# Performance work log

Hardware: AMD Instinct MI355X
Metric: run time of the kernel (lower is better)

The kernel has to match this reference:

```python
import jax, jax.numpy as jnp
import numpy as np

ALPHA = 1.0  # default alpha in the torch forward


def local_patches(x, patch_size):
    """Replicates F.unfold(kernel=p, pad=p//2, stride=1) for x of shape [N,1,H,W].
    Returns [N, p*p, H, W]; patch index is row-major over (kh, kw), matching
    torch.unfold's channel-major/kernel row-major layout (C=1 here)."""
    N, C, H, W = x.shape
    pad = patch_size // 2
    xp = jnp.pad(x, ((0, 0), (0, 0), (pad, pad), (pad, pad)))
    # fixed small loop over the p*p kernel offsets (p=3 -> 9 slices)
    shifts = [xp[:, :, i:i + H, j:j + W]
              for i in range(patch_size) for j in range(patch_size)]
    return jnp.concatenate(shifts, axis=1)  # [N, p*p, H, W]


def setup_inputs() -> dict:
    key = jax.random.key(0)
    x_rgb = jax.random.uniform(key, (8, 3, 512, 512), dtype=jnp.float32)
    return {"x_rgb": x_rgb, "patch_size": 3}


def reference(x_rgb, patch_size):
    # scale_factor=1 -> interpolate is identity
    r = x_rgb[:, 0:1]  # [N,1,H,W]
    g = x_rgb[:, 1:2]
    b = x_rgb[:, 2:3]
    l_channel = 0.2126 * r + 0.7152 * g + 0.0722 * b

    local_r = local_patches(r, patch_size)  # [N,9,H,W]
    local_g = local_patches(g, patch_size)
    local_b = local_patches(b, patch_size)
    local_l = 0.2126 * local_r + 0.7152 * local_g + 0.0722 * local_b

    local_difference_l = (local_l - l_channel) ** 2
    correlation = jax.nn.softmax(-local_difference_l / ALPHA, axis=1)  # [N,9,H,W]

    out_r = jnp.sum(correlation * local_r, axis=1, keepdims=True)
    out_g = jnp.sum(correlation * local_g, axis=1, keepdims=True)
    out_b = jnp.sum(correlation * local_b, axis=1, keepdims=True)
    return jnp.concatenate((out_r, out_g, out_b), axis=1)  # [N,3,H,W]
```

## Files before the change

### kernel.cpp

```cpp
#include <hip/hip_runtime.h>


#define HH 512
#define WW 512
#define HWSZ (HH * WW)

__global__ __launch_bounds__(256) void wavg_kernel(const float* __restrict__ x,
                                                   float* __restrict__ out,
                                                   int total ) {
    int idx = blockIdx.x * 256 + threadIdx.x;
    if (idx >= total) return;

    int n   = idx >> 18;
    int rem = idx & (HWSZ - 1);
    int h   = rem >> 9;
    int w   = rem & (WW - 1);

    const float* Rp = x + (size_t)n * 3 * HWSZ;
    const float* Gp = Rp + HWSZ;
    const float* Bp = Gp + HWSZ;

    float rc = Rp[rem], gc = Gp[rem], bc = Bp[rem];
    float lc = 0.2126f * rc + 0.7152f * gc + 0.0722f * bc;

    float sw = 0.f, sr = 0.f, sg = 0.f, sb = 0.f;

#pragma unroll
    for (int dy = -1; dy <= 1; ++dy) {
#pragma unroll
        for (int dx = -1; dx <= 1; ++dx) {
            int hh = h + dy, ww = w + dx;
            bool inb = ((unsigned)hh < HH) & ((unsigned)ww < WW);
            int i2 = (hh << 9) + ww;
            float rn = 0.f, gn = 0.f, bn = 0.f;
            if (inb) {
                rn = Rp[i2];
                gn = Gp[i2];
                bn = Bp[i2];
            }
            float ln = 0.2126f * rn + 0.7152f * gn + 0.0722f * bn;
            float d  = ln - lc;
            float wt = __expf(-d * d);
            sw += wt;
            sr += wt * rn;
            sg += wt * gn;
            sb += wt * bn;
        }
    }

    float inv = __builtin_amdgcn_rcpf(sw);
    float* Orp = out + (size_t)n * 3 * HWSZ;
    Orp[rem]            = sr * inv;
    Orp[rem + HWSZ]     = sg * inv;
    Orp[rem + 2 * HWSZ] = sb * inv;
}

extern "C" void kernel_launch(void* const* d_in, const int* in_sizes, int n_in,
                              void* d_out, int out_size, void* d_ws, size_t ws_size,
                              hipStream_t stream) {
    const float* x = (const float*)d_in[0];
    float* out = (float*)d_out;
    int total = in_sizes[0] / 3;
    int blocks = (total + 255) / 256;
    wavg_kernel<<<blocks, 256, 0, stream>>>(x, out, total);
}
```

Before: 21.58 us.

## Process eight pixels per thread with row-wise float4 loads and lane shuffles

Each wave now handles one full image row, with each thread computing eight consecutive pixels. The thread loads the three neighbouring rows with vectorized float4 loads and gets its left and right halo pixels from adjacent lanes through shuffles. Luma is computed once per loaded pixel and reused across the overlapping 3x3 windows, and outputs are written with float4 stores. This cuts per-pixel scalar load instructions and redundant luma math, but raises register use and cuts the thread count eightfold.

After: 34.14 us. 1.58x slower.

```diff
diff --git a/kernel.cpp b/kernel.cpp
--- a/kernel.cpp
+++ b/kernel.cpp
@@ -5,54 +5,97 @@
 #define WW 512
 #define HWSZ (HH * WW)
 
+__device__ __forceinline__ float luma(float r, float g, float b) {
+    return 0.2126f * r + 0.7152f * g + 0.0722f * b;
+}
+
 __global__ __launch_bounds__(256) void wavg_kernel(const float* __restrict__ x,
-                                                   float* __restrict__ out,
-                                                   int total ) {
-    int idx = blockIdx.x * 256 + threadIdx.x;
-    if (idx >= total) return;
+                                                   float* __restrict__ out) {
+    const int lane = threadIdx.x & 63;
+    const int wid  = threadIdx.x >> 6;
+    const int row  = (blockIdx.x << 2) + wid;
+    const int n    = row >> 9;
+    const int h    = row & (HH - 1);
+    const int w0   = lane << 3;
 
-    int n   = idx >> 18;
-    int rem = idx & (HWSZ - 1);
-    int h   = rem >> 9;
-    int w   = rem & (WW - 1);
+    const float* __restrict__ base = x + (size_t)n * 3 * HWSZ;
 
-    const float* Rp = x + (size_t)n * 3 * HWSZ;
-    const float* Gp = Rp + HWSZ;
-    const float* Bp = Gp + HWSZ;
+    float sw[8], sr[8], sg[8], sb[8], lc[8];
+#pragma unroll
+    for (int i = 0; i < 8; ++i) { sw[i] = 0.f; sr[i] = 0.f; sg[i] = 0.f; sb[i] = 0.f; }
 
-    float rc = Rp[rem], gc = Gp[rem], bc = Bp[rem];
-    float lc = 0.2126f * rc + 0.7152f * gc + 0.0722f * bc;
+    auto do_row = [&](int hh, bool set_lc) {
+        const bool inb = (unsigned)hh < HH;
+        const float* Rp = base + (inb ? hh : 0) * WW + w0;
+        const float4 z = make_float4(0.f, 0.f, 0.f, 0.f);
+        float4 r0 = inb ? *(const float4*)(Rp)              : z;
+        float4 r1 = inb ? *(const float4*)(Rp + 4)          : z;
+        float4 g0 = inb ? *(const float4*)(Rp + HWSZ)       : z;
+        float4 g1 = inb ? *(const float4*)(Rp + HWSZ + 4)   : z;
+        float4 b0 = inb ? *(const float4*)(Rp + 2*HWSZ)     : z;
+        float4 b1 = inb ? *(const float4*)(Rp + 2*HWSZ + 4) : z;
 
-    float sw = 0.f, sr = 0.f, sg = 0.f, sb = 0.f;
+        float rr[10], gg[10], bb[10], ll[10];
+        rr[1]=r0.x; rr[2]=r0.y; rr[3]=r0.z; rr[4]=r0.w;
+        rr[5]=r1.x; rr[6]=r1.y; rr[7]=r1.z; rr[8]=r1.w;
+        gg[1]=g0.x; gg[2]=g0.y; gg[3]=g0.z; gg[4]=g0.w;
+        gg[5]=g1.x; gg[6]=g1.y; gg[7]=g1.z; gg[8]=g1.w;
+        bb[1]=b0.x; bb[2]=b0.y; bb[3]=b0.z; bb[4]=b0.w;
+        bb[5]=b1.x; bb[6]=b1.y; bb[7]=b1.z; bb[8]=b1.w;
+
+        float rL = __shfl_up(r1.w, 1);   if (lane == 0)  rL = 0.f;
+        float gL = __shfl_up(g1.w, 1);   if (lane == 0)  gL = 0.f;
+        float bL = __shfl_up(b1.w, 1);   if (lane == 0)  bL = 0.f;
+        float rR = __shfl_down(r0.x, 1); if (lane == 63) rR = 0.f;
+        float gR = __shfl_down(g0.x, 1); if (lane == 63) gR = 0.f;
+        float bR = __shfl_down(b0.x, 1); if (lane == 63) bR = 0.f;
+        rr[0] = rL; gg[0] = gL; bb[0] = bL;
+        rr[9] = rR; gg[9] = gR; bb[9] = bR;
 
 #pragma unroll
-    for (int dy = -1; dy <= 1; ++dy) {
+        for (int t = 0; t < 10; ++t) ll[t] = luma(rr[t], gg[t], bb[t]);
+
+        if (set_lc) {
 #pragma unroll
-        for (int dx = -1; dx <= 1; ++dx) {
-            int hh = h + dy, ww = w + dx;
-            bool inb = ((unsigned)hh < HH) & ((unsigned)ww < WW);
-            int i2 = (hh << 9) + ww;
-            float rn = 0.f, gn = 0.f, bn = 0.f;
-            if (inb) {
-                rn = Rp[i2];
-                gn = Gp[i2];
-                bn = Bp[i2];
+            for (int i = 0; i < 8; ++i) lc[i] = ll[i + 1];
+        }
+
+#pragma unroll
+        for (int i = 0; i < 8; ++i) {
+#pragma unroll
+            for (int t = i; t < i + 3; ++t) {
+                float d  = ll[t] - lc[i];
+                float wt = __expf(-d * d);
+                sw[i] += wt;
+                sr[i] += wt * rr[t];
+                sg[i] += wt * gg[t];
+                sb[i] += wt * bb[t];
             }
-            float ln = 0.2126f * rn + 0.7152f * gn + 0.0722f * bn;
-            float d  = ln - lc;
-            float wt = __expf(-d * d);
-            sw += wt;
-            sr += wt * rn;
-            sg += wt * gn;
-            sb += wt * bn;
         }
-    }
+    };
 
-    float inv = __builtin_amdgcn_rcpf(sw);
-    float* Orp = out + (size_t)n * 3 * HWSZ;
-    Orp[rem]            = sr * inv;
-    Orp[rem + HWSZ]     = sg * inv;
-    Orp[rem + 2 * HWSZ] = sb * inv;
+    do_row(h, true);
+    do_row(h - 1, false);
+    do_row(h + 1, false);
+
+    float inv[8];
+#pragma unroll
+    for (int i = 0; i < 8; ++i) inv[i] = __builtin_amdgcn_rcpf(sw[i]);
+
+    float* Op = out + (size_t)n * 3 * HWSZ + h * WW + w0;
+    float4 o0, o1;
+    o0.x = sr[0]*inv[0]; o0.y = sr[1]*inv[1]; o0.z = sr[2]*inv[2]; o0.w = sr[3]*inv[3];
+    o1.x = sr[4]*inv[4]; o1.y = sr[5]*inv[5]; o1.z = sr[6]*inv[6]; o1.w = sr[7]*inv[7];
+    *(float4*)(Op)     = o0;
+    *(float4*)(Op + 4) = o1;
+    o0.x = sg[0]*inv[0]; o0.y = sg[1]*inv[1]; o0.z = sg[2]*inv[2]; o0.w = sg[3]*inv[3];
+    o1.x = sg[4]*inv[4]; o1.y = sg[5]*inv[5]; o1.z = sg[6]*inv[6]; o1.w = sg[7]*inv[7];
+    *(float4*)(Op + HWSZ)     = o0;
+    *(float4*)(Op + HWSZ + 4) = o1;
+    o0.x = sb[0]*inv[0]; o0.y = sb[1]*inv[1]; o0.z = sb[2]*inv[2]; o0.w = sb[3]*inv[3];
+    o1.x = sb[4]*inv[4]; o1.y = sb[5]*inv[5]; o1.z = sb[6]*inv[6]; o1.w = sb[7]*inv[7];
+    *(float4*)(Op + 2*HWSZ)     = o0;
+    *(float4*)(Op + 2*HWSZ + 4) = o1;
 }
 
 extern "C" void kernel_launch(void* const* d_in, const int* in_sizes, int n_in,
@@ -60,7 +103,8 @@
                               hipStream_t stream) {
     const float* x = (const float*)d_in[0];
     float* out = (float*)d_out;
-    int total = in_sizes[0] / 3;
-    int blocks = (total + 255) / 256;
-    wavg_kernel<<<blocks, 256, 0, stream>>>(x, out, total);
+    int nimg   = in_sizes[0] / (3 * HWSZ);
+    int rows   = nimg * HH;
+    int blocks = rows / 4;
+    wavg_kernel<<<blocks, 256, 0, stream>>>(x, out);
 }
```

## Compute four horizontal pixels per thread with vectorized row loads and stores

Applied to the files above, without the earlier changes.

Each thread now handles four adjacent pixels in a row. It loads a float4 plus two halo scalars for each of three rows and three channels, then reuses those loaded neighbours across the four outputs. Results are written as float4 nontemporal stores. The aim is fewer load instructions and less redundant neighbour traffic per pixel, at the cost of more registers per thread and a quarter as many threads. Boundary handling moves from branches to clamped indices with multiplicative masks.

Result: faster. 20.65 us, median of 2 (-4.3%).

```diff
diff --git a/kernel.cpp b/kernel.cpp
--- a/kernel.cpp
+++ b/kernel.cpp
@@ -5,54 +5,106 @@
 #define WW 512
 #define HWSZ (HH * WW)
 
-__global__ __launch_bounds__(256) void wavg_kernel(const float* __restrict__ x,
-                                                   float* __restrict__ out,
-                                                   int total ) {
-    int idx = blockIdx.x * 256 + threadIdx.x;
-    if (idx >= total) return;
+typedef float f32x4 __attribute__((ext_vector_type(4)));
 
-    int n   = idx >> 18;
-    int rem = idx & (HWSZ - 1);
-    int h   = rem >> 9;
-    int w   = rem & (WW - 1);
+__device__ __forceinline__ float luma(float r, float g, float b) {
+    return 0.2126f * r + 0.7152f * g + 0.0722f * b;
+}
 
-    const float* Rp = x + (size_t)n * 3 * HWSZ;
-    const float* Gp = Rp + HWSZ;
-    const float* Bp = Gp + HWSZ;
+__device__ __forceinline__ void load6(const float* __restrict__ p, int w0,
+                                      int wlC, int wrC, float m, float mL,
+                                      float mR, float o[6]) {
+    f32x4 v  = *(const f32x4*)(p + w0);
+    float lv = p[wlC];
+    float rv = p[wrC];
+    o[0] = lv * mL;
+    o[1] = v.x * m; o[2] = v.y * m; o[3] = v.z * m; o[4] = v.w * m;
+    o[5] = rv * mR;
+}
 
-    float rc = Rp[rem], gc = Gp[rem], bc = Bp[rem];
-    float lc = 0.2126f * rc + 0.7152f * gc + 0.0722f * bc;
-
-    float sw = 0.f, sr = 0.f, sg = 0.f, sb = 0.f;
-
+__device__ __forceinline__ void accum(const float rr[6], const float gg[6],
+                                      const float bb[6], const float lc[4],
+                                      float sw[4], float sr[4], float sg[4],
+                                      float sb[4]) {
+    float ll[6];
 #pragma unroll
-    for (int dy = -1; dy <= 1; ++dy) {
+    for (int t = 0; t < 6; ++t) ll[t] = luma(rr[t], gg[t], bb[t]);
 #pragma unroll
-        for (int dx = -1; dx <= 1; ++dx) {
-            int hh = h + dy, ww = w + dx;
-            bool inb = ((unsigned)hh < HH) & ((unsigned)ww < WW);
-            int i2 = (hh << 9) + ww;
-            float rn = 0.f, gn = 0.f, bn = 0.f;
-            if (inb) {
-                rn = Rp[i2];
-                gn = Gp[i2];
-                bn = Bp[i2];
-            }
-            float ln = 0.2126f * rn + 0.7152f * gn + 0.0722f * bn;
-            float d  = ln - lc;
+    for (int i = 0; i < 4; ++i) {
+#pragma unroll
+        for (int t = i; t < i + 3; ++t) {
+            float d  = ll[t] - lc[i];
             float wt = __expf(-d * d);
-            sw += wt;
-            sr += wt * rn;
-            sg += wt * gn;
-            sb += wt * bn;
+            sw[i] += wt;
+            sr[i] += wt * rr[t];
+            sg[i] += wt * gg[t];
+            sb[i] += wt * bb[t];
         }
     }
+}
 
-    float inv = __builtin_amdgcn_rcpf(sw);
-    float* Orp = out + (size_t)n * 3 * HWSZ;
-    Orp[rem]            = sr * inv;
-    Orp[rem + HWSZ]     = sg * inv;
-    Orp[rem + 2 * HWSZ] = sb * inv;
+__global__ __launch_bounds__(256) void wavg_kernel(const float* __restrict__ x,
+                                                   float* __restrict__ out) {
+    const int gid = blockIdx.x * 256 + threadIdx.x;
+    const int w0  = (gid & 127) << 2;
+    const int row = gid >> 7;
+    const int n   = row >> 9;
+    const int h   = row & (HH - 1);
+
+    const float* __restrict__ base = x + (size_t)n * 3 * HWSZ;
+
+    const int   wlC = (w0 > 0) ? w0 - 1 : 0;
+    const int   wrC = (w0 + 4 < WW) ? w0 + 4 : WW - 1;
+    const float mkL = (w0 > 0) ? 1.f : 0.f;
+    const float mkR = (w0 + 4 < WW) ? 1.f : 0.f;
+
+    const int   hmC = (h > 0) ? h - 1 : 0;
+    const int   hpC = (h < HH - 1) ? h + 1 : HH - 1;
+    const float mM  = (h > 0) ? 1.f : 0.f;
+    const float mP  = (h < HH - 1) ? 1.f : 0.f;
+
+    float rc[6], gc[6], bc[6];
+    float rm[6], gm[6], bm[6];
+    float rp[6], gp[6], bp[6];
+    load6(base + 0 * HWSZ + h * WW,   w0, wlC, wrC, 1.f, mkL,      mkR,      rc);
+    load6(base + 1 * HWSZ + h * WW,   w0, wlC, wrC, 1.f, mkL,      mkR,      gc);
+    load6(base + 2 * HWSZ + h * WW,   w0, wlC, wrC, 1.f, mkL,      mkR,      bc);
+    load6(base + 0 * HWSZ + hmC * WW, w0, wlC, wrC, mM,  mM * mkL, mM * mkR, rm);
+    load6(base + 1 * HWSZ + hmC * WW, w0, wlC, wrC, mM,  mM * mkL, mM * mkR, gm);
+    load6(base + 2 * HWSZ + hmC * WW, w0, wlC, wrC, mM,  mM * mkL, mM * mkR, bm);
+    load6(base + 0 * HWSZ + hpC * WW, w0, wlC, wrC, mP,  mP * mkL, mP * mkR, rp);
+    load6(base + 1 * HWSZ + hpC * WW, w0, wlC, wrC, mP,  mP * mkL, mP * mkR, gp);
+    load6(base + 2 * HWSZ + hpC * WW, w0, wlC, wrC, mP,  mP * mkL, mP * mkR, bp);
+
+    float lc[4];
+    {
+        float llc[6];
+#pragma unroll
+        for (int t = 0; t < 6; ++t) llc[t] = luma(rc[t], gc[t], bc[t]);
+#pragma unroll
+        for (int i = 0; i < 4; ++i) lc[i] = llc[i + 1];
+    }
+
+    float sw[4], sr[4], sg[4], sb[4];
+#pragma unroll
+    for (int i = 0; i < 4; ++i) { sw[i] = 0.f; sr[i] = 0.f; sg[i] = 0.f; sb[i] = 0.f; }
+
+    accum(rc, gc, bc, lc, sw, sr, sg, sb);
+    accum(rm, gm, bm, lc, sw, sr, sg, sb);
+    accum(rp, gp, bp, lc, sw, sr, sg, sb);
+
+    float inv[4];
+#pragma unroll
+    for (int i = 0; i < 4; ++i) inv[i] = __builtin_amdgcn_rcpf(sw[i]);
+
+    float* Op = out + (size_t)n * 3 * HWSZ + h * WW + w0;
+    f32x4 o;
+    o.x = sr[0]*inv[0]; o.y = sr[1]*inv[1]; o.z = sr[2]*inv[2]; o.w = sr[3]*inv[3];
+    __builtin_nontemporal_store(o, (f32x4*)(Op));
+    o.x = sg[0]*inv[0]; o.y = sg[1]*inv[1]; o.z = sg[2]*inv[2]; o.w = sg[3]*inv[3];
+    __builtin_nontemporal_store(o, (f32x4*)(Op + HWSZ));
+    o.x = sb[0]*inv[0]; o.y = sb[1]*inv[1]; o.z = sb[2]*inv[2]; o.w = sb[3]*inv[3];
+    __builtin_nontemporal_store(o, (f32x4*)(Op + 2 * HWSZ));
 }
 
 extern "C" void kernel_launch(void* const* d_in, const int* in_sizes, int n_in,
@@ -60,7 +112,7 @@
                               hipStream_t stream) {
     const float* x = (const float*)d_in[0];
     float* out = (float*)d_out;
-    int total = in_sizes[0] / 3;
+    int total  = in_sizes[0] / (3 * 4);
     int blocks = (total + 255) / 256;
-    wavg_kernel<<<blocks, 256, 0, stream>>>(x, out, total);
+    wavg_kernel<<<blocks, 256, 0, stream>>>(x, out);
 }
```
